# Optimization experiments

Hardware: AMD Instinct MI355X
Metric: run time of the kernel (lower is better)

Reference implementation:

```python
import jax, jax.numpy as jnp
import numpy as np

N = 500_000
N_ATOMS = 5
T = 8                # angle triplets per (residue, bead) table row
CONT_LEN = 36
GATE_OFFSET = 1
NUM_EXPERTS = 18
BEAD_COL = 36
MAX_BEADS = 4
ANGLE_WEIGHT = 1.0
EPS = 1e-8
MIN_LEN = 0.02


def setup_inputs() -> dict:
    key = jax.random.key(0)
    ks = jax.random.split(key, 8)
    x = jax.random.uniform(ks[0], (N, 38), dtype=jnp.float32)
    # gate column holds residue id in [1, num_experts]; bead column in [0, max_beads)
    res = jax.random.randint(ks[1], (N,), 1, NUM_EXPERTS + 1).astype(jnp.float32)
    bead = jax.random.randint(ks[2], (N,), 0, MAX_BEADS).astype(jnp.float32)
    x = x.at[:, CONT_LEN + 1].set(res)
    x = x.at[:, BEAD_COL].set(bead)
    y_true = jax.random.normal(ks[3], (N, N_ATOMS * 3), dtype=jnp.float32)
    y_pred = jax.random.normal(ks[4], (N, N_ATOMS * 3), dtype=jnp.float32)
    mask = (jax.random.uniform(ks[5], (N, N_ATOMS * 3)) < 0.85).astype(jnp.float32)
    # -1 entries act as invalid-triplet sentinels (trip_ok branch)
    trip = jax.random.randint(ks[6], (NUM_EXPERTS, MAX_BEADS, T, 3), -1, N_ATOMS, dtype=jnp.int32)
    valid = jax.random.randint(ks[7], (NUM_EXPERTS, MAX_BEADS, T), 0, 2, dtype=jnp.int32)
    return {"x": x, "y_true": y_true, "y_pred": y_pred, "mask": mask,
            "angle_triplets_table": trip, "angle_valid_table": valid}


def _atom_mse(true, pred, m):
    # masked per-atom squared error, normalized by count of valid atoms per sample
    se_atom = jnp.sum(jnp.square(true - pred) * m, axis=-1)          # [N, A]
    atom_valid = jnp.any(m > 0.0, axis=-1).astype(se_atom.dtype)     # [N, A]
    num = jnp.sum(se_atom * atom_valid, axis=-1)
    den = jnp.sum(atom_valid, axis=-1) + EPS
    return jnp.mean(num / den)


def _angle_loss(x, true, pred, m, trip_table, valid_table):
    gate = x[:, CONT_LEN + 1]
    gate = jnp.where(jnp.isfinite(gate), gate, 0.0)
    res_id = jnp.clip(jnp.round(gate).astype(jnp.int32) - GATE_OFFSET, 0, NUM_EXPERTS - 1)
    bead = x[:, BEAD_COL]
    bead = jnp.where(jnp.isfinite(bead), bead, 0.0)
    bead_id = jnp.clip(jnp.round(bead).astype(jnp.int32), 0, MAX_BEADS - 1)

    atom_valid = jnp.any(m > 0.0, axis=-1)                           # [N, A]
    trip = trip_table[res_id, bead_id]                               # [N, T, 3]
    base_valid = valid_table[res_id, bead_id]                        # [N, T]
    trip_ok = jnp.all(trip >= 0, axis=-1)
    ts = jnp.maximum(trip, 0)
    i_idx, j_idx, k_idx = ts[..., 0], ts[..., 1], ts[..., 2]         # [N, T]

    rows = jnp.arange(true.shape[0])[:, None]
    vi = atom_valid[rows, i_idx]
    vj = atom_valid[rows, j_idx]
    vk = atom_valid[rows, k_idx]
    ti, tj, tk = true[rows, i_idx], true[rows, j_idx], true[rows, k_idx]   # [N, T, 3]
    pi, pj, pk = pred[rows, i_idx], pred[rows, j_idx], pred[rows, k_idx]

    v1t, v2t, v1p, v2p = ti - tj, tk - tj, pi - pj, pk - pj
    ml2 = jnp.float32(MIN_LEN * MIN_LEN)
    sq = lambda v: jnp.sum(jnp.square(v), axis=-1)
    l1t2, l2t2, l1p2, l2p2 = sq(v1t), sq(v2t), sq(v1p), sq(v2p)

    valid = (trip_ok & (base_valid > 0) & vi & vj & vk
             & (l1t2 > ml2) & (l2t2 > ml2) & (l1p2 > ml2) & (l2p2 > ml2))

    unit = lambda v, l2: v * jax.lax.rsqrt(jnp.maximum(l2, ml2))[..., None]
    u1t, u2t = unit(v1t, l1t2), unit(v2t, l2t2)
    u1p, u2p = unit(v1p, l1p2), unit(v2p, l2p2)

    clip = lambda c: jnp.clip(c, -1.0 + 1e-6, 1.0 - 1e-6)
    cos_t = clip(jnp.sum(u1t * u2t, axis=-1))
    cos_p = clip(jnp.sum(u1p * u2p, axis=-1))
    sin_t = jnp.linalg.norm(jnp.cross(u1t, u2t), axis=-1)
    sin_p = jnp.linalg.norm(jnp.cross(u1p, u2p), axis=-1)

    per_ang = jnp.square(cos_p - cos_t) + jnp.square(sin_p - sin_t)
    per_ang = jnp.where(valid, per_ang, 0.0)
    num = jnp.sum(per_ang, axis=-1)
    den = jnp.sum(valid.astype(jnp.float32), axis=-1) + EPS
    return jnp.mean(num / den)


def reference(x, y_true, y_pred, mask, angle_triplets_table, angle_valid_table):
    true = y_true.reshape(-1, N_ATOMS, 3).astype(jnp.float32)
    pred = y_pred.reshape(-1, N_ATOMS, 3).astype(jnp.float32)
    m = mask.reshape(-1, N_ATOMS, 3).astype(jnp.float32)
    atom = _atom_mse(true, pred, m)
    ang = _angle_loss(x, true, pred, m, angle_triplets_table, angle_valid_table)
    return atom + ANGLE_WEIGHT * ang
```

## Files before the change

kernel.cpp:

```cpp
#include <hip/hip_runtime.h>
#include <math.h>

#define NATOMS 5
#define NEXP 18
#define NBEAD 4
#define EPSV 1e-8f
#define ML2 (0.02f * 0.02f)

__global__ void pack_tables(const int* __restrict__ trip, const int* __restrict__ valid,
                            int4* __restrict__ ptbl) {
    int c = blockIdx.x * blockDim.x + threadIdx.x;
    if (c < NEXP * NBEAD) {
        unsigned w[4] = {0u, 0u, 0u, 0u};
#pragma unroll
        for (int t = 0; t < 8; t++) {
            int b = c * 8 + t;
            int i = trip[b * 3 + 0], j = trip[b * 3 + 1], k = trip[b * 3 + 2];
            unsigned ok = (i >= 0 && j >= 0 && k >= 0 && valid[b] > 0) ? 1u : 0u;
            unsigned oi = 3u * (unsigned)min(max(i, 0), NATOMS - 1);
            unsigned oj = 3u * (unsigned)min(max(j, 0), NATOMS - 1);
            unsigned ov = 3u * (unsigned)min(max(k, 0), NATOMS - 1);
            unsigned e = oi | (oj << 4) | (ov << 8) | (ok << 12);
            w[t >> 1] |= e << ((t & 1) * 16);
        }
        ptbl[c] = make_int4((int)w[0], (int)w[1], (int)w[2], (int)w[3]);
    }
}

__device__ __forceinline__ float row_loss(const float* __restrict__ T,
                                          const float* __restrict__ P,
                                          unsigned mbits, int4 pk, float* __restrict__ st) {
    float num_a = 0.f, den_a = 0.f;
    unsigned avm2 = 0u;
#pragma unroll
    for (int a = 0; a < 5; a++) {
        unsigned mb = (mbits >> (3 * a)) & 7u;
        float d0 = T[3 * a + 0] - P[3 * a + 0];
        float d1 = T[3 * a + 1] - P[3 * a + 1];
        float d2 = T[3 * a + 2] - P[3 * a + 2];
        float se = (mb & 1u ? d0 * d0 : 0.f) + (mb & 2u ? d1 * d1 : 0.f) +
                   (mb & 4u ? d2 * d2 : 0.f);
        if (mb) { num_a += se; den_a += 1.f; avm2 |= 1u << (3 * a); }
    }
    float res = num_a / (den_a + EPSV);

#pragma unroll
    for (int c = 0; c < 15; c++) st[c] = T[c];
#pragma unroll
    for (int c = 0; c < 15; c++) st[16 + c] = P[c];

    unsigned tw0 = (unsigned)pk.x, tw1 = (unsigned)pk.y;
    unsigned tw2 = (unsigned)pk.z, tw3 = (unsigned)pk.w;

    float num_g = 0.f, den_g = 0.f;
#pragma unroll
    for (int t = 0; t < 8; t++) {
        unsigned wrd = (t < 2) ? tw0 : (t < 4) ? tw1 : (t < 6) ? tw2 : tw3;
        unsigned e = (wrd >> ((t & 1) * 16)) & 0xffffu;
        int oi = e & 15, oj = (e >> 4) & 15, ov = (e >> 8) & 15;
        bool wok = ((e >> 12) & 1u) != 0u;

        float tix = st[oi], tiy = st[oi + 1], tiz = st[oi + 2];
        float tjx = st[oj], tjy = st[oj + 1], tjz = st[oj + 2];
        float tkx = st[ov], tky = st[ov + 1], tkz = st[ov + 2];
        float pix = st[16 + oi], piy = st[17 + oi], piz = st[18 + oi];
        float pjx = st[16 + oj], pjy = st[17 + oj], pjz = st[18 + oj];
        float pkx = st[16 + ov], pky = st[17 + ov], pkz = st[18 + ov];

        float v1tx = tix - tjx, v1ty = tiy - tjy, v1tz = tiz - tjz;
        float v2tx = tkx - tjx, v2ty = tky - tjy, v2tz = tkz - tjz;
        float v1px = pix - pjx, v1py = piy - pjy, v1pz = piz - pjz;
        float v2px = pkx - pjx, v2py = pky - pjy, v2pz = pkz - pjz;

        float l1t = fmaf(v1tx, v1tx, fmaf(v1ty, v1ty, v1tz * v1tz));
        float l2t = fmaf(v2tx, v2tx, fmaf(v2ty, v2ty, v2tz * v2tz));
        float l1p = fmaf(v1px, v1px, fmaf(v1py, v1py, v1pz * v1pz));
        float l2p = fmaf(v2px, v2px, fmaf(v2py, v2py, v2pz * v2pz));

        bool okv = wok && ((avm2 >> oi) & 1) && ((avm2 >> oj) & 1) &&
                   ((avm2 >> ov) & 1) && (l1t > ML2) && (l2t > ML2) &&
                   (l1p > ML2) && (l2p > ML2);

        float rt = __builtin_amdgcn_rsqf(fmaxf(l1t, ML2) * fmaxf(l2t, ML2));
        float rp = __builtin_amdgcn_rsqf(fmaxf(l1p, ML2) * fmaxf(l2p, ML2));

        float dott = fmaf(v1tx, v2tx, fmaf(v1ty, v2ty, v1tz * v2tz));
        float dotp = fmaf(v1px, v2px, fmaf(v1py, v2py, v1pz * v2pz));
        float cut = dott * rt;
        float cup = dotp * rp;
        float cost = fminf(fmaxf(cut, -1.f + 1e-6f), 1.f - 1e-6f);
        float cosp = fminf(fmaxf(cup, -1.f + 1e-6f), 1.f - 1e-6f);
        float sint = __builtin_amdgcn_sqrtf(fmaxf(fmaf(-cut, cut, 1.f), 0.f));
        float sinp = __builtin_amdgcn_sqrtf(fmaxf(fmaf(-cup, cup, 1.f), 0.f));

        float dc = cosp - cost, dsn = sinp - sint;
        if (okv) { num_g += fmaf(dc, dc, dsn * dsn); den_g += 1.f; }
    }
    return res + num_g / (den_g + EPSV);
}

__global__ __launch_bounds__(256, 4) void loss_kernel(
    const float* __restrict__ xin, const float* __restrict__ y_true,
    const float* __restrict__ y_pred, const float* __restrict__ mask,
    const int4* __restrict__ ptbl, float* __restrict__ partial, int n) {
    __shared__ float scr[256 * 33];

    const int tid = threadIdx.x;
    const int row0 = blockIdx.x * 512 + tid;
    const int row1 = row0 + 256;
    const bool v0 = row0 < n, v1 = row1 < n;
    float* st = scr + tid * 33;

    float T0[15], P0[15], T1[15], P1[15];
    unsigned mb0 = 0u, mb1 = 0u;
    float2 gb0 = make_float2(0.f, 0.f), gb1 = make_float2(0.f, 0.f);

    if (v0) {
        const size_t rb = (size_t)row0 * 15;
#pragma unroll
        for (int c = 0; c < 15; c++) T0[c] = y_true[rb + c];
#pragma unroll
        for (int c = 0; c < 15; c++) P0[c] = y_pred[rb + c];
        gb0 = *(const float2*)(xin + (size_t)row0 * 38 + 36);
        float M0[15];
#pragma unroll
        for (int c = 0; c < 15; c++) M0[c] = mask[rb + c];
#pragma unroll
        for (int c = 0; c < 15; c++) mb0 |= (M0[c] > 0.f ? 1u : 0u) << c;
    }
    if (v1) {
        const size_t rb = (size_t)row1 * 15;
#pragma unroll
        for (int c = 0; c < 15; c++) T1[c] = y_true[rb + c];
#pragma unroll
        for (int c = 0; c < 15; c++) P1[c] = y_pred[rb + c];
        gb1 = *(const float2*)(xin + (size_t)row1 * 38 + 36);
        float M1[15];
#pragma unroll
        for (int c = 0; c < 15; c++) M1[c] = mask[rb + c];
#pragma unroll
        for (int c = 0; c < 15; c++) mb1 |= (M1[c] > 0.f ? 1u : 0u) << c;
    }

    int4 pk0 = make_int4(0, 0, 0, 0), pk1 = make_int4(0, 0, 0, 0);
    if (v0) {
        float beadf = isfinite(gb0.x) ? gb0.x : 0.f;
        float gatef = isfinite(gb0.y) ? gb0.y : 0.f;
        gatef = fminf(fmaxf(gatef, -1e6f), 1e6f);
        beadf = fminf(fmaxf(beadf, -1e6f), 1e6f);
        int rid = min(max((int)rintf(gatef) - 1, 0), NEXP - 1);
        int bid = min(max((int)rintf(beadf), 0), NBEAD - 1);
        pk0 = ptbl[rid * NBEAD + bid];
    }
    if (v1) {
        float beadf = isfinite(gb1.x) ? gb1.x : 0.f;
        float gatef = isfinite(gb1.y) ? gb1.y : 0.f;
        gatef = fminf(fmaxf(gatef, -1e6f), 1e6f);
        beadf = fminf(fmaxf(beadf, -1e6f), 1e6f);
        int rid = min(max((int)rintf(gatef) - 1, 0), NEXP - 1);
        int bid = min(max((int)rintf(beadf), 0), NBEAD - 1);
        pk1 = ptbl[rid * NBEAD + bid];
    }

    float result = 0.f;
    if (v0) result += row_loss(T0, P0, mb0, pk0, st);
    if (v1) result += row_loss(T1, P1, mb1, pk1, st);

#pragma unroll
    for (int off = 32; off > 0; off >>= 1)
        result += __shfl_down(result, off, 64);
    __syncthreads();
    float* red = scr;
    int lane = tid & 63, wv = tid >> 6;
    if (lane == 0) red[wv] = result;
    __syncthreads();
    if (tid == 0) partial[blockIdx.x] = red[0] + red[1] + red[2] + red[3];
}

__global__ __launch_bounds__(256) void reduce_kernel(const float* __restrict__ partial,
                                                     float* __restrict__ out, int nblocks,
                                                     float inv_n) {
    __shared__ float red[4];
    float s = 0.f;
    for (int i = threadIdx.x; i < nblocks; i += 256) s += partial[i];
#pragma unroll
    for (int off = 32; off > 0; off >>= 1) s += __shfl_down(s, off, 64);
    int lane = threadIdx.x & 63, wv = threadIdx.x >> 6;
    if (lane == 0) red[wv] = s;
    __syncthreads();
    if (threadIdx.x == 0) out[0] = (red[0] + red[1] + red[2] + red[3]) * inv_n;
}

extern "C" void kernel_launch(void* const* d_in, const int* in_sizes, int n_in,
                              void* d_out, int out_size, void* d_ws, size_t ws_size,
                              hipStream_t stream) {
    const float* x = (const float*)d_in[0];
    const float* y_true = (const float*)d_in[1];
    const float* y_pred = (const float*)d_in[2];
    const float* mask = (const float*)d_in[3];
    const int* trip = (const int*)d_in[4];
    const int* valid = (const int*)d_in[5];
    float* out = (float*)d_out;

    int4* ptbl = (int4*)d_ws;
    float* partial = (float*)((char*)d_ws + 4096);

    const int n = in_sizes[1] / 15;
    const int blocks = (n + 511) / 512;

    pack_tables<<<1, 128, 0, stream>>>(trip, valid, ptbl);
    loss_kernel<<<blocks, 256, 0, stream>>>(x, y_true, y_pred, mask, ptbl, partial, n);
    reduce_kernel<<<1, 256, 0, stream>>>(partial, out, blocks, 1.0f / (float)n);
}
```

Measured before the change: 194.5 us.

## Process four rows per thread with 16-byte vector nontemporal loads in single-wave blocks

Each thread now handles four consecutive rows, so it can read its 60 floats of y_true, y_pred and mask as 15 aligned float4 nontemporal loads rather than 15 scalar loads per row. Blocks shrink to one 64-thread wave, which removes the shared-memory cross-wave reduction and its barriers. The aim is fewer, wider memory transactions on this bandwidth-bound kernel. In exchange, register pressure rises sharply (T[60], P[60], Mv[15]), which may cut occupancy. The tail is guarded only by base < n, so it assumes n is a multiple of 4.

```diff
diff --git a/kernel.cpp b/kernel.cpp
--- a/kernel.cpp
+++ b/kernel.cpp
@@ -6,6 +6,9 @@
 #define NBEAD 4
 #define EPSV 1e-8f
 #define ML2 (0.02f * 0.02f)
+
+typedef float vf4a __attribute__((ext_vector_type(4), aligned(16)));
+typedef float vf2u __attribute__((ext_vector_type(2), aligned(4)));
 
 __global__ void pack_tables(const int* __restrict__ trip, const int* __restrict__ valid,
                             int4* __restrict__ ptbl) {
@@ -99,82 +102,78 @@
     return res + num_g / (den_g + EPSV);
 }
 
-__global__ __launch_bounds__(256, 4) void loss_kernel(
+__global__ __launch_bounds__(64, 2) void loss_kernel(
     const float* __restrict__ xin, const float* __restrict__ y_true,
     const float* __restrict__ y_pred, const float* __restrict__ mask,
     const int4* __restrict__ ptbl, float* __restrict__ partial, int n) {
-    __shared__ float scr[256 * 33];
+    __shared__ float scr[64 * 33];
 
     const int tid = threadIdx.x;
-    const int row0 = blockIdx.x * 512 + tid;
-    const int row1 = row0 + 256;
-    const bool v0 = row0 < n, v1 = row1 < n;
+    const int base = blockIdx.x * 256 + tid * 4;
     float* st = scr + tid * 33;
 
-    float T0[15], P0[15], T1[15], P1[15];
-    unsigned mb0 = 0u, mb1 = 0u;
-    float2 gb0 = make_float2(0.f, 0.f), gb1 = make_float2(0.f, 0.f);
-
-    if (v0) {
-        const size_t rb = (size_t)row0 * 15;
-#pragma unroll
-        for (int c = 0; c < 15; c++) T0[c] = y_true[rb + c];
-#pragma unroll
-        for (int c = 0; c < 15; c++) P0[c] = y_pred[rb + c];
-        gb0 = *(const float2*)(xin + (size_t)row0 * 38 + 36);
-        float M0[15];
-#pragma unroll
-        for (int c = 0; c < 15; c++) M0[c] = mask[rb + c];
-#pragma unroll
-        for (int c = 0; c < 15; c++) mb0 |= (M0[c] > 0.f ? 1u : 0u) << c;
-    }
-    if (v1) {
-        const size_t rb = (size_t)row1 * 15;
-#pragma unroll
-        for (int c = 0; c < 15; c++) T1[c] = y_true[rb + c];
-#pragma unroll
-        for (int c = 0; c < 15; c++) P1[c] = y_pred[rb + c];
-        gb1 = *(const float2*)(xin + (size_t)row1 * 38 + 36);
-        float M1[15];
-#pragma unroll
-        for (int c = 0; c < 15; c++) M1[c] = mask[rb + c];
-#pragma unroll
-        for (int c = 0; c < 15; c++) mb1 |= (M1[c] > 0.f ? 1u : 0u) << c;
-    }
-
-    int4 pk0 = make_int4(0, 0, 0, 0), pk1 = make_int4(0, 0, 0, 0);
-    if (v0) {
-        float beadf = isfinite(gb0.x) ? gb0.x : 0.f;
-        float gatef = isfinite(gb0.y) ? gb0.y : 0.f;
-        gatef = fminf(fmaxf(gatef, -1e6f), 1e6f);
-        beadf = fminf(fmaxf(beadf, -1e6f), 1e6f);
-        int rid = min(max((int)rintf(gatef) - 1, 0), NEXP - 1);
-        int bid = min(max((int)rintf(beadf), 0), NBEAD - 1);
-        pk0 = ptbl[rid * NBEAD + bid];
-    }
-    if (v1) {
-        float beadf = isfinite(gb1.x) ? gb1.x : 0.f;
-        float gatef = isfinite(gb1.y) ? gb1.y : 0.f;
-        gatef = fminf(fmaxf(gatef, -1e6f), 1e6f);
-        beadf = fminf(fmaxf(beadf, -1e6f), 1e6f);
-        int rid = min(max((int)rintf(gatef) - 1, 0), NEXP - 1);
-        int bid = min(max((int)rintf(beadf), 0), NBEAD - 1);
-        pk1 = ptbl[rid * NBEAD + bid];
-    }
-
     float result = 0.f;
-    if (v0) result += row_loss(T0, P0, mb0, pk0, st);
-    if (v1) result += row_loss(T1, P1, mb1, pk1, st);
+    if (base < n) {
+        const size_t gb = (size_t)base * 15;
+        const vf4a* qT = (const vf4a*)(y_true + gb);
+        const vf4a* qP = (const vf4a*)(y_pred + gb);
+        const vf4a* qM = (const vf4a*)(mask + gb);
+
+        float T[60], P[60];
+        vf4a Mv[15];
+#pragma unroll
+        for (int k = 0; k < 15; k++) {
+            vf4a t = __builtin_nontemporal_load(qT + k);
+            T[4 * k + 0] = t.x; T[4 * k + 1] = t.y; T[4 * k + 2] = t.z; T[4 * k + 3] = t.w;
+        }
+#pragma unroll
+        for (int k = 0; k < 15; k++) {
+            vf4a p = __builtin_nontemporal_load(qP + k);
+            P[4 * k + 0] = p.x; P[4 * k + 1] = p.y; P[4 * k + 2] = p.z; P[4 * k + 3] = p.w;
+        }
+#pragma unroll
+        for (int k = 0; k < 15; k++) Mv[k] = __builtin_nontemporal_load(qM + k);
+
+        vf2u gbv[4];
+#pragma unroll
+        for (int r = 0; r < 4; r++)
+            gbv[r] = __builtin_nontemporal_load(
+                (const vf2u*)(xin + (size_t)(base + r) * 38 + 36));
+
+        unsigned mb[4] = {0u, 0u, 0u, 0u};
+#pragma unroll
+        for (int k = 0; k < 15; k++) {
+#pragma unroll
+            for (int c = 0; c < 4; c++) {
+                int e = 4 * k + c;
+                int r = e / 15, p = e - r * 15;
+                float m = (c == 0) ? Mv[k].x : (c == 1) ? Mv[k].y : (c == 2) ? Mv[k].z
+                                                                             : Mv[k].w;
+                mb[r] |= (m > 0.f ? 1u : 0u) << p;
+            }
+        }
+
+        int4 pk[4];
+#pragma unroll
+        for (int r = 0; r < 4; r++) {
+            float beadf = isfinite(gbv[r].x) ? gbv[r].x : 0.f;
+            float gatef = isfinite(gbv[r].y) ? gbv[r].y : 0.f;
+            gatef = fminf(fmaxf(gatef, -1e6f), 1e6f);
+            beadf = fminf(fmaxf(beadf, -1e6f), 1e6f);
+            int rid = min(max((int)rintf(gatef) - 1, 0), NEXP - 1);
+            int bid = min(max((int)rintf(beadf), 0), NBEAD - 1);
+            pk[r] = ptbl[rid * NBEAD + bid];
+        }
+
+#pragma unroll
+        for (int r = 0; r < 4; r++)
+            result += row_loss(T + 15 * r, P + 15 * r, mb[r], pk[r], st);
+    }
 
 #pragma unroll
     for (int off = 32; off > 0; off >>= 1)
         result += __shfl_down(result, off, 64);
-    __syncthreads();
-    float* red = scr;
-    int lane = tid & 63, wv = tid >> 6;
-    if (lane == 0) red[wv] = result;
-    __syncthreads();
-    if (tid == 0) partial[blockIdx.x] = red[0] + red[1] + red[2] + red[3];
+    if (tid == 0) partial[blockIdx.x] = result;
 }
 
 __global__ __launch_bounds__(256) void reduce_kernel(const float* __restrict__ partial,
@@ -206,9 +205,9 @@
     float* partial = (float*)((char*)d_ws + 4096);
 
     const int n = in_sizes[1] / 15;
-    const int blocks = (n + 511) / 512;
+    const int blocks = (n + 255) / 256;
 
     pack_tables<<<1, 128, 0, stream>>>(trip, valid, ptbl);
-    loss_kernel<<<blocks, 256, 0, stream>>>(x, y_true, y_pred, mask, ptbl, partial, n);
+    loss_kernel<<<blocks, 64, 0, stream>>>(x, y_true, y_pred, mask, ptbl, partial, n);
     reduce_kernel<<<1, 256, 0, stream>>>(partial, out, blocks, 1.0f / (float)n);
 }
```

Result: slower. 215.8 us (+10.9%).
